# Kernel tuning notes

Measured on AMD Instinct MI355X. Metric: run time of the kernel, lower is better.

Reference implementation:

```python
import jax, jax.numpy as jnp
import numpy as np
from jax import lax


def _phi(x):
    # feature map phi(x) = elu(x) + 1 (non-negative)
    return jax.nn.elu(x) + 1.0


def setup_inputs() -> dict:
    key = jax.random.key(0)
    ks = jax.random.split(key, 5)
    B, T, D, H = 8, 4096, 1024, 64
    x = jax.random.normal(ks[0], (B, T, D), dtype=jnp.float32)
    # torch Linear(d_model, d_head, bias=False): y = x @ W.T; store as (in, out)
    W_q = jax.random.normal(ks[1], (D, H), dtype=jnp.float32) * (1.0 / np.sqrt(D))
    W_k = jax.random.normal(ks[2], (D, H), dtype=jnp.float32) * (1.0 / np.sqrt(D))
    W_v = jax.random.normal(ks[3], (D, H), dtype=jnp.float32) * (1.0 / np.sqrt(D))
    W_o = jax.random.normal(ks[4], (H, D), dtype=jnp.float32) * (1.0 / np.sqrt(H))
    return {"x": x, "W_q": W_q, "W_k": W_k, "W_v": W_v, "W_o": W_o}


def reference(x, W_q, W_k, W_v, W_o):
    B, T, D = x.shape
    H = W_q.shape[1]
    q = _phi(jnp.einsum('btd,dh->bth', x, W_q))  # [B,T,H]
    k = _phi(jnp.einsum('btd,dh->bth', x, W_k))
    v = jnp.einsum('btd,dh->bth', x, W_v)

    # time-major for scan: [T,B,H]
    qT = jnp.swapaxes(q, 0, 1)
    kT = jnp.swapaxes(k, 0, 1)
    vT = jnp.swapaxes(v, 0, 1)

    S0 = jnp.zeros((B, H, H), dtype=x.dtype)
    z0 = jnp.zeros((B, H), dtype=x.dtype)

    def step(carry, inp):
        S, z = carry
        q_t, k_t, v_t = inp
        S = S + k_t[:, :, None] * v_t[:, None, :]   # S += phi(k) v^T
        z = z + k_t
        o_t = jnp.einsum('bij,bj->bi', S, q_t)       # matches torch einsum exactly
        denom = jnp.maximum(jnp.sum(z * q_t, axis=-1, keepdims=True), 1e-6)
        return (S, z), o_t / denom

    (_, _), oT = lax.scan(step, (S0, z0), (qT, kT, vT))  # oT: [T,B,H]
    o = jnp.swapaxes(oT, 0, 1)                            # [B,T,H]
    # dropout is identity at inference
    return jnp.einsum('bth,hd->btd', o, W_o)
```

## Files before the change

### kernel.cpp

```cpp
#include <hip/hip_runtime.h>
#include <math.h>

typedef float4 f4;
typedef __attribute__((ext_vector_type(4))) float f32x4;
typedef __attribute__((ext_vector_type(8))) short short8;
typedef __attribute__((ext_vector_type(4))) unsigned short u16x4;

static constexpr int kB  = 8;
static constexpr int kT  = 4096;
static constexpr int kD  = 1024;
static constexpr int kH  = 64;
static constexpr int kC  = 64;
static constexpr int kNC = kT / kC;
static constexpr long kBT = (long)kB * kT;

__device__ __forceinline__ float phi_f(float x) {
    return x > 0.0f ? x + 1.0f : __expf(x);
}

__device__ __forceinline__ unsigned short f2bf(float f) {
    unsigned int u = __float_as_uint(f);
    u += 0x7FFF + ((u >> 16) & 1);
    return (unsigned short)(u >> 16);
}

typedef const __attribute__((address_space(1))) unsigned int gu32;
typedef __attribute__((address_space(3))) unsigned int lu32;
#define GLL16(SRC, DST) __builtin_amdgcn_global_load_lds((gu32*)(SRC), (lu32*)(DST), 16, 0, 0)

#define LD4F(dst, src) { f4 _t_ = *(const f4*)(src); (dst)[0]=_t_.x; (dst)[1]=_t_.y; (dst)[2]=_t_.z; (dst)[3]=_t_.w; }

__global__ __launch_bounds__(256)
void k0_prep(const float* __restrict__ Wq, const float* __restrict__ Wk,
             const float* __restrict__ Wv, const float* __restrict__ Wo,
             unsigned short* __restrict__ Wg, unsigned short* __restrict__ Wot)
{
    int g = blockIdx.x * 256 + threadIdx.x;
    if (g < 24576) {
        int r   = g % 192;
        int rem = g / 192;
        int c   = rem & 3;
        int kt  = rem >> 2;
        int mat = r >> 6, nn = r & 63;
        const float* W = (mat == 0) ? Wq : ((mat == 1) ? Wk : Wv);
        int kbase = kt * 32 + c * 8;
        unsigned short* dst = Wg + (long)g * 8;
        #pragma unroll
        for (int e = 0; e < 8; ++e) dst[e] = f2bf(W[(long)(kbase + e) * kH + nn]);
    } else if (g < 24576 + 4096) {
        int g2 = g - 24576;
        int n  = g2 >> 2;
        int kc = (g2 & 3) * 16;
        unsigned short* dst = Wot + n * kH + kc;
        #pragma unroll
        for (int i = 0; i < 16; ++i) dst[i] = f2bf(Wo[(long)(kc + i) * kD + n]);
    }
}

__global__ __launch_bounds__(256, 2)
void k1_qkv_mfma(const float* __restrict__ x, const unsigned short* __restrict__ Wg,
                 float* __restrict__ q, float* __restrict__ k, float* __restrict__ v)
{
    __shared__ unsigned short Bs[2][6144];
    __shared__ unsigned short As[2][2048];

    const int t = threadIdx.x;
    const int w = t >> 6;
    const int l = t & 63;
    const long mb = (long)blockIdx.x * 64;

    const int arow = t >> 2;
    const int ac   = t & 3;
    const float* ap = x + (mb + arow) * kD + ac * 8;
    const int awoff = (ac * 64 + arow) * 8;

    const int fc = l >> 4;
    const int fr = l & 15;

    f32x4 acc[12];
    #pragma unroll
    for (int i = 0; i < 12; ++i) acc[i] = (f32x4){0.f, 0.f, 0.f, 0.f};

    #pragma unroll
    for (int c3 = 0; c3 < 3; ++c3) {
        int idx = w * 3 + c3;
        GLL16(Wg + idx * 512 + l * 8, &Bs[0][idx * 512]);
    }
    f32x4 a0 = *(const f32x4*)ap;
    f32x4 a1 = *(const f32x4*)(ap + 4);
    {
        short8 ab;
        ab[0] = (short)f2bf(a0[0]); ab[1] = (short)f2bf(a0[1]);
        ab[2] = (short)f2bf(a0[2]); ab[3] = (short)f2bf(a0[3]);
        ab[4] = (short)f2bf(a1[0]); ab[5] = (short)f2bf(a1[1]);
        ab[6] = (short)f2bf(a1[2]); ab[7] = (short)f2bf(a1[3]);
        *(short8*)&As[0][awoff] = ab;
    }
    a0 = *(const f32x4*)(ap + 32);
    a1 = *(const f32x4*)(ap + 36);
    __syncthreads();

    for (int kt = 0; kt < 32; ++kt) {
        const int cur = kt & 1, nxt = cur ^ 1;
        if (kt + 1 < 32) {
            #pragma unroll
            for (int c3 = 0; c3 < 3; ++c3) {
                int idx = w * 3 + c3;
                GLL16(Wg + (long)(kt + 1) * 6144 + idx * 512 + l * 8, &Bs[nxt][idx * 512]);
            }
            short8 ab;
            ab[0] = (short)f2bf(a0[0]); ab[1] = (short)f2bf(a0[1]);
            ab[2] = (short)f2bf(a0[2]); ab[3] = (short)f2bf(a0[3]);
            ab[4] = (short)f2bf(a1[0]); ab[5] = (short)f2bf(a1[1]);
            ab[6] = (short)f2bf(a1[2]); ab[7] = (short)f2bf(a1[3]);
            *(short8*)&As[nxt][awoff] = ab;
            if (kt + 2 < 32) {
                a0 = *(const f32x4*)(ap + (kt + 2) * 32);
                a1 = *(const f32x4*)(ap + (kt + 2) * 32 + 4);
            }
        }
        short8 af = *(const short8*)&As[cur][(fc * 64 + w * 16 + fr) * 8];
        #pragma unroll
        for (int n16 = 0; n16 < 12; ++n16) {
            short8 bf = *(const short8*)&Bs[cur][(fc * 192 + n16 * 16 + fr) * 8];
            acc[n16] = __builtin_amdgcn_mfma_f32_16x16x32_bf16(af, bf, acc[n16], 0, 0, 0);
        }
        __syncthreads();
    }

    const int om = (l >> 4) * 4;
    #pragma unroll
    for (int n16 = 0; n16 < 12; ++n16) {
        int mat = n16 >> 2;
        int col = (n16 & 3) * 16 + (l & 15);
        float* outp = (mat == 0) ? q : ((mat == 1) ? k : v);
        #pragma unroll
        for (int reg = 0; reg < 4; ++reg) {
            long row = mb + w * 16 + om + reg;
            float val = acc[n16][reg];
            if (mat < 2) val = phi_f(val);
            outp[row * kH + col] = val;
        }
    }
}

__global__ __launch_bounds__(256)
void k2_state(const float* __restrict__ k, const float* __restrict__ v,
              float* __restrict__ Sc, float* __restrict__ zc)
{
    __shared__ float Ks2[64][64];
    __shared__ float Vs2[64][64];
    const int t = threadIdx.x;
    const long bc = blockIdx.x;
    const long rowbase = bc * kC;

    #pragma unroll
    for (int i = 0; i < 4; ++i) {
        int fi  = t + i * 256;
        int tau = fi >> 4;
        int cc  = (fi & 15) * 4;
        *(f4*)&Ks2[tau][cc] = *(const f4*)&k[(rowbase + tau) * kH + cc];
        *(f4*)&Vs2[tau][cc] = *(const f4*)&v[(rowbase + tau) * kH + cc];
    }
    __syncthreads();

    const int i  = t >> 2;
    const int j0 = (t & 3) * 16;
    float acc[16];
    #pragma unroll
    for (int c = 0; c < 16; ++c) acc[c] = 0.0f;
    float zacc = 0.0f;

    for (int tau = 0; tau < 64; ++tau) {
        float kv = Ks2[tau][i];
        zacc += kv;
        #pragma unroll
        for (int c = 0; c < 4; ++c) {
            float vv[4];
            LD4F(vv, &Vs2[tau][j0 + c * 4]);
            #pragma unroll
            for (int e = 0; e < 4; ++e) acc[c * 4 + e] += kv * vv[e];
        }
    }
    float* scp = Sc + bc * (kH * kH) + i * kH + j0;
    #pragma unroll
    for (int c = 0; c < 4; ++c) {
        f4 val; val.x = acc[c*4]; val.y = acc[c*4+1]; val.z = acc[c*4+2]; val.w = acc[c*4+3];
        *(f4*)&scp[c * 4] = val;
    }
    if ((t & 3) == 0) zc[bc * kH + i] = zacc;
}

__global__ __launch_bounds__(256)
void k3_prefix(const float* __restrict__ Sc, float* __restrict__ Sp,
               const float* __restrict__ zc, float* __restrict__ zp)
{
    const int t = threadIdx.x;
    const int blk = blockIdx.x;
    if (blk < 128) {
        int g = blk * 256 + t;
        int b = g >> 12;
        int rem = g & 4095;
        const float* src = Sc + (long)b * kNC * kH * kH + rem;
        float*       dst = Sp + (long)b * kNC * kH * kH + rem;
        float vals[kNC];
        #pragma unroll
        for (int c = 0; c < kNC; ++c) vals[c] = src[c * (kH * kH)];
        float run = 0.0f;
        #pragma unroll
        for (int c = 0; c < kNC; ++c) { float nv = vals[c]; vals[c] = run; run += nv; }
        #pragma unroll
        for (int c = 0; c < kNC; ++c) dst[c * (kH * kH)] = vals[c];
    } else {
        int g = (blk - 128) * 256 + t;
        int b = g >> 6;
        int i = g & 63;
        const float* src = zc + (long)b * kNC * kH + i;
        float*       dst = zp + (long)b * kNC * kH + i;
        float vals[kNC];
        #pragma unroll
        for (int c = 0; c < kNC; ++c) vals[c] = src[c * kH];
        float run = 0.0f;
        #pragma unroll
        for (int c = 0; c < kNC; ++c) { float nv = vals[c]; vals[c] = run; run += nv; }
        #pragma unroll
        for (int c = 0; c < kNC; ++c) dst[c * kH] = vals[c];
    }
}

__global__ __launch_bounds__(256)
void k4_chunkout(const float* __restrict__ q, const float* __restrict__ k,
                 const float* __restrict__ v, const float* __restrict__ Sp,
                 const float* __restrict__ zp, unsigned short* __restrict__ o)
{
    __shared__ float QT[64 * 64];
    __shared__ float KsS[64 * 64];
    __shared__ float VT[64 * 64];
    __shared__ float zps[64];
    __shared__ float ds[64];

    const int t = threadIdx.x;
    const long bc = blockIdx.x;
    const long rowbase = bc * kC;

    #pragma unroll
    for (int ii = 0; ii < 4; ++ii) {
        int fi  = t + ii * 256;
        int tau = fi >> 4;
        int c4  = fi & 15;
        f4 qv = *(const f4*)&q[(rowbase + tau) * kH + c4 * 4];
        QT[(c4 * 4 + 0) * 64 + tau] = qv.x;
        QT[(c4 * 4 + 1) * 64 + tau] = qv.y;
        QT[(c4 * 4 + 2) * 64 + tau] = qv.z;
        QT[(c4 * 4 + 3) * 64 + tau] = qv.w;
        f4 vv = *(const f4*)&v[(rowbase + tau) * kH + c4 * 4];
        VT[(c4 * 4 + 0) * 64 + tau] = vv.x;
        VT[(c4 * 4 + 1) * 64 + tau] = vv.y;
        VT[(c4 * 4 + 2) * 64 + tau] = vv.z;
        VT[(c4 * 4 + 3) * 64 + tau] = vv.w;
        f4 kv = *(const f4*)&k[(rowbase + tau) * kH + c4 * 4];
        *(f4*)&KsS[tau * 64 + 4 * (c4 ^ (tau & 15))] = kv;
    }
    if (t < 16) {
        *(f4*)&zps[t * 4] = *(const f4*)&zp[bc * kH + t * 4];
    }
    __syncthreads();

    const int tg   = t & 15;
    const int ig   = t >> 4;
    const int tau0 = tg * 4;
    const int ip0  = ig * 4;

    float pv[4][4];
    #pragma unroll
    for (int a = 0; a < 4; ++a)
        #pragma unroll
        for (int b2 = 0; b2 < 4; ++b2) pv[a][b2] = 0.0f;
    for (int xx = 0; xx < 64; ++xx) {
        float q4[4], v4[4];
        LD4F(q4, &QT[xx * 64 + tau0]);
        LD4F(v4, &VT[xx * 64 + ip0]);
        #pragma unroll
        for (int e1 = 0; e1 < 4; ++e1)
            #pragma unroll
            for (int e0 = 0; e0 < 4; ++e0) pv[e1][e0] += v4[e1] * q4[e0];
    }
    __syncthreads();
    #pragma unroll
    for (int e1 = 0; e1 < 4; ++e1) {
        int tp = ip0 + e1;
        f4 w;
        w.x = (tp <= tau0 + 0) ? pv[e1][0] : 0.0f;
        w.y = (tp <= tau0 + 1) ? pv[e1][1] : 0.0f;
        w.z = (tp <= tau0 + 2) ? pv[e1][2] : 0.0f;
        w.w = (tp <= tau0 + 3) ? pv[e1][3] : 0.0f;
        *(f4*)&VT[tp * 64 + tau0] = w;
    }
    __syncthreads();

    float acc[4][4];
    #pragma unroll
    for (int a = 0; a < 4; ++a)
        #pragma unroll
        for (int b2 = 0; b2 < 4; ++b2) acc[a][b2] = 0.0f;
    for (int tp = 0; tp < 64; ++tp) {
        float p4[4], k4[4];
        LD4F(p4, &VT[tp * 64 + tau0]);
        LD4F(k4, &KsS[tp * 64 + 4 * (ig ^ (tp & 15))]);
        #pragma unroll
        for (int e0 = 0; e0 < 4; ++e0)
            #pragma unroll
            for (int e1 = 0; e1 < 4; ++e1) acc[e0][e1] += p4[e0] * k4[e1];
    }
    __syncthreads();

    #pragma unroll
    for (int ii = 0; ii < 4; ++ii) {
        int fi = t + ii * 256;
        int ir = fi >> 4;
        int j4 = fi & 15;
        f4 sv = *(const f4*)&Sp[bc * (kH * kH) + ir * kH + j4 * 4];
        VT[(j4 * 4 + 0) * 64 + ir] = sv.x;
        VT[(j4 * 4 + 1) * 64 + ir] = sv.y;
        VT[(j4 * 4 + 2) * 64 + ir] = sv.z;
        VT[(j4 * 4 + 3) * 64 + ir] = sv.w;
    }
    if (t < 64) {
        float run = 0.0f;
        const int jc4 = t >> 2, jr = t & 3;
        for (int tau = 0; tau < 64; ++tau) {
            int idx = tau * 64 + 4 * (jc4 ^ (tau & 15)) + jr;
            run += KsS[idx];
            KsS[idx] = run;
        }
    }
    __syncthreads();

    if (t < 64) {
        float dacc = 0.0f;
        for (int j = 0; j < 64; ++j) {
            float qv = QT[j * 64 + t];
            float ck = KsS[t * 64 + 4 * ((j >> 2) ^ (t & 15)) + (j & 3)];
            dacc += qv * (ck + zps[j]);
        }
        ds[t] = 1.0f / fmaxf(dacc, 1e-6f);
    }

    for (int j = 0; j < 64; ++j) {
        float q4[4], s4[4];
        LD4F(q4, &QT[j * 64 + tau0]);
        LD4F(s4, &VT[j * 64 + ip0]);
        #pragma unroll
        for (int e0 = 0; e0 < 4; ++e0)
            #pragma unroll
            for (int e1 = 0; e1 < 4; ++e1) acc[e0][e1] += q4[e0] * s4[e1];
    }
    __syncthreads();

    #pragma unroll
    for (int e0 = 0; e0 < 4; ++e0) {
        float inv = ds[tau0 + e0];
        u16x4 wv;
        wv[0] = f2bf(acc[e0][0] * inv);
        wv[1] = f2bf(acc[e0][1] * inv);
        wv[2] = f2bf(acc[e0][2] * inv);
        wv[3] = f2bf(acc[e0][3] * inv);
        *(u16x4*)&o[(rowbase + tau0 + e0) * kH + ip0] = wv;
    }
}

__global__ __launch_bounds__(256, 4)
void k5_outproj_mfma(const unsigned short* __restrict__ o,
                     const unsigned short* __restrict__ Wot,
                     float* __restrict__ out)
{
    __shared__ unsigned short Os[128 * 64];
    __shared__ unsigned short Ws5[128 * 64];
    const int t = threadIdx.x;
    const int w = t >> 6, l = t & 63;
    const int wm = w >> 1, wn = w & 1;
    const int mb = blockIdx.x >> 3;
    const int nb = blockIdx.x & 7;
    const long row0 = (long)mb * 128;
    const int  col0 = nb * 128;

    const int rin = l >> 3;
    const int cch = l & 7;
    #pragma unroll
    for (int c = 0; c < 4; ++c) {
        int r = (c * 4 + w) * 8 + rin;
        int g = cch ^ (r & 7);
        GLL16(o   + (row0 + r) * kH + g * 8,        Os  + (c * 4 + w) * 512);
        GLL16(Wot + (long)(col0 + r) * kH + g * 8,  Ws5 + (c * 4 + w) * 512);
    }
    __syncthreads();

    short8 af[4][2];
    #pragma unroll
    for (int mf = 0; mf < 4; ++mf) {
        int ar = wm * 64 + mf * 16 + (l & 15);
        #pragma unroll
        for (int ks = 0; ks < 2; ++ks)
            af[mf][ks] = *(const short8*)(Os + ar * 64 + (((ks * 4 + (l >> 4)) ^ (ar & 7)) * 8));
    }

    f32x4 acc[4][4];
    #pragma unroll
    for (int a = 0; a < 4; ++a)
        #pragma unroll
        for (int b2 = 0; b2 < 4; ++b2) acc[a][b2] = (f32x4){0.f, 0.f, 0.f, 0.f};

    #pragma unroll
    for (int nf = 0; nf < 4; ++nf) {
        int br = wn * 64 + nf * 16 + (l & 15);
        short8 bf0 = *(const short8*)(Ws5 + br * 64 + ((((l >> 4)) ^ (br & 7)) * 8));
        short8 bf1 = *(const short8*)(Ws5 + br * 64 + (((4 + (l >> 4)) ^ (br & 7)) * 8));
        #pragma unroll
        for (int mf = 0; mf < 4; ++mf) {
            acc[mf][nf] = __builtin_amdgcn_mfma_f32_16x16x32_bf16(af[mf][0], bf0, acc[mf][nf], 0, 0, 0);
            acc[mf][nf] = __builtin_amdgcn_mfma_f32_16x16x32_bf16(af[mf][1], bf1, acc[mf][nf], 0, 0, 0);
        }
    }

    #pragma unroll
    for (int mf = 0; mf < 4; ++mf)
        #pragma unroll
        for (int nf = 0; nf < 4; ++nf) {
            #pragma unroll
            for (int reg = 0; reg < 4; ++reg) {
                long row = row0 + wm * 64 + mf * 16 + (l >> 4) * 4 + reg;
                int  col = col0 + wn * 64 + nf * 16 + (l & 15);
                out[row * kD + col] = acc[mf][nf][reg];
            }
        }
}

extern "C" void kernel_launch(void* const* d_in, const int* in_sizes, int n_in,
                              void* d_out, int out_size, void* d_ws, size_t ws_size,
                              hipStream_t stream)
{
    const float* x  = (const float*)d_in[0];
    const float* Wq = (const float*)d_in[1];
    const float* Wk = (const float*)d_in[2];
    const float* Wv = (const float*)d_in[3];
    const float* Wo = (const float*)d_in[4];
    float* out = (float*)d_out;
    float* ws  = (float*)d_ws;

    const long NQ = kBT * kH;
    float* q  = ws;
    float* k  = ws + NQ;
    float* v  = ws + 2 * NQ;
    float* Sc = ws + 3 * NQ;
    float* Sp = ws + 4 * NQ;
    unsigned short* obf = (unsigned short*)(ws + 5 * NQ);
    float* zc = ws + 5 * NQ + NQ / 2;
    float* zp = zc + (long)kB * kNC * kH;
    unsigned short* Wg  = (unsigned short*)(zp + (long)kB * kNC * kH);
    unsigned short* Wot = Wg + 192 * 1024;

    k0_prep<<<112, 256, 0, stream>>>(Wq, Wk, Wv, Wo, Wg, Wot);
    k1_qkv_mfma<<<512, 256, 0, stream>>>(x, Wg, q, k, v);
    k2_state<<<kB * kNC, 256, 0, stream>>>(k, v, Sc, zc);
    k3_prefix<<<130, 256, 0, stream>>>(Sc, Sp, zc, zp);
    k4_chunkout<<<kB * kNC, 256, 0, stream>>>(q, k, v, Sp, zp, obf);
    k5_outproj_mfma<<<2048, 256, 0, stream>>>(obf, Wot, out);
}
```

Before: 307.3 us.

## Rewrite intra-chunk output kernel with bf16 MFMA and split-bf16 prefix state

The chunk output kernel, previously scalar FP32 FMAs over LDS, is replaced by bf16 MFMA matmuls for QK^T, QV^T-style masked products and Q·S. The QKV projection kernel now also emits bf16 copies of q/k/v and a transposed k tile. The prefix-sum kernel writes the state as a high/low bf16 pair to keep it close to fp32 precision. Inputs are staged into LDS with direct global-to-LDS loads. In exchange the intra-chunk terms run in bf16 (accuracy risk), and the extra bf16 buffers add memory writes.

```diff
diff --git a/kernel.cpp b/kernel.cpp
--- a/kernel.cpp
+++ b/kernel.cpp
@@ -4,7 +4,7 @@
 typedef float4 f4;
 typedef __attribute__((ext_vector_type(4))) float f32x4;
 typedef __attribute__((ext_vector_type(8))) short short8;
-typedef __attribute__((ext_vector_type(4))) unsigned short u16x4;
+typedef __attribute__((ext_vector_type(8))) unsigned short u16x8;
 
 static constexpr int kB  = 8;
 static constexpr int kT  = 4096;
@@ -22,6 +22,10 @@
     unsigned int u = __float_as_uint(f);
     u += 0x7FFF + ((u >> 16) & 1);
     return (unsigned short)(u >> 16);
+}
+
+__device__ __forceinline__ float bf2f(unsigned short u) {
+    return __uint_as_float((unsigned int)u << 16);
 }
 
 typedef const __attribute__((address_space(1))) unsigned int gu32;
@@ -59,7 +63,10 @@
 
 __global__ __launch_bounds__(256, 2)
 void k1_qkv_mfma(const float* __restrict__ x, const unsigned short* __restrict__ Wg,
-                 float* __restrict__ q, float* __restrict__ k, float* __restrict__ v)
+                 unsigned short* __restrict__ qb,
+                 float* __restrict__ kf, unsigned short* __restrict__ kb,
+                 float* __restrict__ vf, unsigned short* __restrict__ vb,
+                 unsigned short* __restrict__ kTg)
 {
     __shared__ unsigned short Bs[2][6144];
     __shared__ unsigned short As[2][2048];
@@ -128,19 +135,39 @@
         __syncthreads();
     }
 
+    unsigned short* kTt = &Bs[0][0];
     const int om = (l >> 4) * 4;
     #pragma unroll
     for (int n16 = 0; n16 < 12; ++n16) {
         int mat = n16 >> 2;
         int col = (n16 & 3) * 16 + (l & 15);
-        float* outp = (mat == 0) ? q : ((mat == 1) ? k : v);
         #pragma unroll
         for (int reg = 0; reg < 4; ++reg) {
-            long row = mb + w * 16 + om + reg;
+            int  row  = w * 16 + om + reg;
+            long grow = mb + row;
             float val = acc[n16][reg];
             if (mat < 2) val = phi_f(val);
-            outp[row * kH + col] = val;
-        }
+            unsigned short bv = f2bf(val);
+            if (mat == 0) {
+                qb[grow * kH + col] = bv;
+            } else if (mat == 1) {
+                kf[grow * kH + col] = val;
+                kb[grow * kH + col] = bv;
+                kTt[col * 72 + row] = bv;
+            } else {
+                vf[grow * kH + col] = val;
+                vb[grow * kH + col] = bv;
+            }
+        }
+    }
+    __syncthreads();
+    {
+        int i = t >> 2, s = (t & 3) * 16;
+        u16x8 h0 = *(const u16x8*)&kTt[i * 72 + s];
+        u16x8 h1 = *(const u16x8*)&kTt[i * 72 + s + 8];
+        unsigned short* dst = kTg + (long)blockIdx.x * 4096 + i * 64 + s;
+        *(u16x8*)dst       = h0;
+        *(u16x8*)(dst + 8) = h1;
     }
 }
 
@@ -192,7 +219,8 @@
 }
 
 __global__ __launch_bounds__(256)
-void k3_prefix(const float* __restrict__ Sc, float* __restrict__ Sp,
+void k3_prefix(const float* __restrict__ Sc,
+               unsigned short* __restrict__ SpH, unsigned short* __restrict__ SpL,
                const float* __restrict__ zc, float* __restrict__ zp)
 {
     const int t = threadIdx.x;
@@ -201,16 +229,21 @@
         int g = blk * 256 + t;
         int b = g >> 12;
         int rem = g & 4095;
-        const float* src = Sc + (long)b * kNC * kH * kH + rem;
-        float*       dst = Sp + (long)b * kNC * kH * kH + rem;
+        const float* src       = Sc  + (long)b * kNC * 4096 + rem;
+        unsigned short* dh     = SpH + (long)b * kNC * 4096 + rem;
+        unsigned short* dl     = SpL + (long)b * kNC * 4096 + rem;
         float vals[kNC];
         #pragma unroll
-        for (int c = 0; c < kNC; ++c) vals[c] = src[c * (kH * kH)];
+        for (int c = 0; c < kNC; ++c) vals[c] = src[c * 4096];
         float run = 0.0f;
         #pragma unroll
         for (int c = 0; c < kNC; ++c) { float nv = vals[c]; vals[c] = run; run += nv; }
         #pragma unroll
-        for (int c = 0; c < kNC; ++c) dst[c * (kH * kH)] = vals[c];
+        for (int c = 0; c < kNC; ++c) {
+            unsigned short h = f2bf(vals[c]);
+            dh[c * 4096] = h;
+            dl[c * 4096] = f2bf(vals[c] - bf2f(h));
+        }
     } else {
         int g = (blk - 128) * 256 + t;
         int b = g >> 6;
@@ -228,144 +261,122 @@
     }
 }
 
-__global__ __launch_bounds__(256)
-void k4_chunkout(const float* __restrict__ q, const float* __restrict__ k,
-                 const float* __restrict__ v, const float* __restrict__ Sp,
-                 const float* __restrict__ zp, unsigned short* __restrict__ o)
-{
-    __shared__ float QT[64 * 64];
-    __shared__ float KsS[64 * 64];
-    __shared__ float VT[64 * 64];
-    __shared__ float zps[64];
-    __shared__ float ds[64];
+__global__ __launch_bounds__(256, 2)
+void k4_chunkout_mfma(const unsigned short* __restrict__ qb,
+                      const unsigned short* __restrict__ kb,
+                      const unsigned short* __restrict__ vb,
+                      const unsigned short* __restrict__ kTg,
+                      const unsigned short* __restrict__ SpH,
+                      const unsigned short* __restrict__ SpL,
+                      const float* __restrict__ zp,
+                      unsigned short* __restrict__ o)
+{
+    __shared__ unsigned short Q[4096], K[4096], V[4096], KT[4096];
+    __shared__ unsigned short SH[4096], SL[4096], Pl[4096];
+    __shared__ float zps[64], qz[64];
 
     const int t = threadIdx.x;
+    const int w = t >> 6, l = t & 63;
     const long bc = blockIdx.x;
-    const long rowbase = bc * kC;
-
-    #pragma unroll
-    for (int ii = 0; ii < 4; ++ii) {
-        int fi  = t + ii * 256;
-        int tau = fi >> 4;
-        int c4  = fi & 15;
-        f4 qv = *(const f4*)&q[(rowbase + tau) * kH + c4 * 4];
-        QT[(c4 * 4 + 0) * 64 + tau] = qv.x;
-        QT[(c4 * 4 + 1) * 64 + tau] = qv.y;
-        QT[(c4 * 4 + 2) * 64 + tau] = qv.z;
-        QT[(c4 * 4 + 3) * 64 + tau] = qv.w;
-        f4 vv = *(const f4*)&v[(rowbase + tau) * kH + c4 * 4];
-        VT[(c4 * 4 + 0) * 64 + tau] = vv.x;
-        VT[(c4 * 4 + 1) * 64 + tau] = vv.y;
-        VT[(c4 * 4 + 2) * 64 + tau] = vv.z;
-        VT[(c4 * 4 + 3) * 64 + tau] = vv.w;
-        f4 kv = *(const f4*)&k[(rowbase + tau) * kH + c4 * 4];
-        *(f4*)&KsS[tau * 64 + 4 * (c4 ^ (tau & 15))] = kv;
-    }
-    if (t < 16) {
-        *(f4*)&zps[t * 4] = *(const f4*)&zp[bc * kH + t * 4];
-    }
-    __syncthreads();
-
-    const int tg   = t & 15;
-    const int ig   = t >> 4;
-    const int tau0 = tg * 4;
-    const int ip0  = ig * 4;
-
-    float pv[4][4];
-    #pragma unroll
-    for (int a = 0; a < 4; ++a)
-        #pragma unroll
-        for (int b2 = 0; b2 < 4; ++b2) pv[a][b2] = 0.0f;
-    for (int xx = 0; xx < 64; ++xx) {
-        float q4[4], v4[4];
-        LD4F(q4, &QT[xx * 64 + tau0]);
-        LD4F(v4, &VT[xx * 64 + ip0]);
-        #pragma unroll
-        for (int e1 = 0; e1 < 4; ++e1)
-            #pragma unroll
-            for (int e0 = 0; e0 < 4; ++e0) pv[e1][e0] += v4[e1] * q4[e0];
-    }
-    __syncthreads();
-    #pragma unroll
-    for (int e1 = 0; e1 < 4; ++e1) {
-        int tp = ip0 + e1;
-        f4 w;
-        w.x = (tp <= tau0 + 0) ? pv[e1][0] : 0.0f;
-        w.y = (tp <= tau0 + 1) ? pv[e1][1] : 0.0f;
-        w.z = (tp <= tau0 + 2) ? pv[e1][2] : 0.0f;
-        w.w = (tp <= tau0 + 3) ? pv[e1][3] : 0.0f;
-        *(f4*)&VT[tp * 64 + tau0] = w;
-    }
-    __syncthreads();
-
-    float acc[4][4];
-    #pragma unroll
-    for (int a = 0; a < 4; ++a)
-        #pragma unroll
-        for (int b2 = 0; b2 < 4; ++b2) acc[a][b2] = 0.0f;
-    for (int tp = 0; tp < 64; ++tp) {
-        float p4[4], k4[4];
-        LD4F(p4, &VT[tp * 64 + tau0]);
-        LD4F(k4, &KsS[tp * 64 + 4 * (ig ^ (tp & 15))]);
-        #pragma unroll
-        for (int e0 = 0; e0 < 4; ++e0)
-            #pragma unroll
-            for (int e1 = 0; e1 < 4; ++e1) acc[e0][e1] += p4[e0] * k4[e1];
-    }
-    __syncthreads();
-
-    #pragma unroll
-    for (int ii = 0; ii < 4; ++ii) {
-        int fi = t + ii * 256;
-        int ir = fi >> 4;
-        int j4 = fi & 15;
-        f4 sv = *(const f4*)&Sp[bc * (kH * kH) + ir * kH + j4 * 4];
-        VT[(j4 * 4 + 0) * 64 + ir] = sv.x;
-        VT[(j4 * 4 + 1) * 64 + ir] = sv.y;
-        VT[(j4 * 4 + 2) * 64 + ir] = sv.z;
-        VT[(j4 * 4 + 3) * 64 + ir] = sv.w;
+    const long base = bc * 4096;
+
+    #pragma unroll
+    for (int j2 = 0; j2 < 2; ++j2) {
+        int j = w * 2 + j2;
+        int off = j * 512 + l * 8;
+        GLL16(qb  + base + off, Q  + j * 512);
+        GLL16(kb  + base + off, K  + j * 512);
+        GLL16(vb  + base + off, V  + j * 512);
+        GLL16(kTg + base + off, KT + j * 512);
+        GLL16(SpH + base + off, SH + j * 512);
+        GLL16(SpL + base + off, SL + j * 512);
+    }
+    if (t < 16) *(f4*)&zps[t * 4] = *(const f4*)&zp[bc * kH + t * 4];
+    __syncthreads();
+
+    const int fr = l & 15, fc = l >> 4;
+    const int aoff = (w * 16 + fr) * 64 + fc * 8;
+
+    f32x4 s_acc[4], p_acc[4];
+    #pragma unroll
+    for (int n16 = 0; n16 < 4; ++n16) {
+        s_acc[n16] = (f32x4){0.f, 0.f, 0.f, 0.f};
+        p_acc[n16] = (f32x4){0.f, 0.f, 0.f, 0.f};
+    }
+    #pragma unroll
+    for (int k32 = 0; k32 < 2; ++k32) {
+        short8 aq = *(const short8*)&Q[aoff + k32 * 32];
+        #pragma unroll
+        for (int n16 = 0; n16 < 4; ++n16) {
+            int boff = (n16 * 16 + fr) * 64 + k32 * 32 + fc * 8;
+            s_acc[n16] = __builtin_amdgcn_mfma_f32_16x16x32_bf16(
+                aq, *(const short8*)&K[boff], s_acc[n16], 0, 0, 0);
+            p_acc[n16] = __builtin_amdgcn_mfma_f32_16x16x32_bf16(
+                aq, *(const short8*)&V[boff], p_acc[n16], 0, 0, 0);
+        }
+    }
+
+    float rsum[4] = {0.f, 0.f, 0.f, 0.f};
+    #pragma unroll
+    for (int n16 = 0; n16 < 4; ++n16) {
+        int col = n16 * 16 + fr;
+        #pragma unroll
+        for (int reg = 0; reg < 4; ++reg) {
+            int row = w * 16 + fc * 4 + reg;
+            bool keep = (col <= row);
+            Pl[row * 64 + col] = keep ? f2bf(p_acc[n16][reg]) : (unsigned short)0;
+            if (keep) rsum[reg] += s_acc[n16][reg];
+        }
+    }
+    #pragma unroll
+    for (int reg = 0; reg < 4; ++reg) {
+        rsum[reg] += __shfl_xor(rsum[reg], 1);
+        rsum[reg] += __shfl_xor(rsum[reg], 2);
+        rsum[reg] += __shfl_xor(rsum[reg], 4);
+        rsum[reg] += __shfl_xor(rsum[reg], 8);
     }
     if (t < 64) {
-        float run = 0.0f;
-        const int jc4 = t >> 2, jr = t & 3;
-        for (int tau = 0; tau < 64; ++tau) {
-            int idx = tau * 64 + 4 * (jc4 ^ (tau & 15)) + jr;
-            run += KsS[idx];
-            KsS[idx] = run;
-        }
-    }
-    __syncthreads();
-
-    if (t < 64) {
-        float dacc = 0.0f;
-        for (int j = 0; j < 64; ++j) {
-            float qv = QT[j * 64 + t];
-            float ck = KsS[t * 64 + 4 * ((j >> 2) ^ (t & 15)) + (j & 3)];
-            dacc += qv * (ck + zps[j]);
-        }
-        ds[t] = 1.0f / fmaxf(dacc, 1e-6f);
-    }
-
-    for (int j = 0; j < 64; ++j) {
-        float q4[4], s4[4];
-        LD4F(q4, &QT[j * 64 + tau0]);
-        LD4F(s4, &VT[j * 64 + ip0]);
-        #pragma unroll
-        for (int e0 = 0; e0 < 4; ++e0)
-            #pragma unroll
-            for (int e1 = 0; e1 < 4; ++e1) acc[e0][e1] += q4[e0] * s4[e1];
-    }
-    __syncthreads();
-
-    #pragma unroll
-    for (int e0 = 0; e0 < 4; ++e0) {
-        float inv = ds[tau0 + e0];
-        u16x4 wv;
-        wv[0] = f2bf(acc[e0][0] * inv);
-        wv[1] = f2bf(acc[e0][1] * inv);
-        wv[2] = f2bf(acc[e0][2] * inv);
-        wv[3] = f2bf(acc[e0][3] * inv);
-        *(u16x4*)&o[(rowbase + tau0 + e0) * kH + ip0] = wv;
+        float accz = 0.0f;
+        #pragma unroll 8
+        for (int j = 0; j < 64; ++j) accz += bf2f(Q[t * 64 + j]) * zps[j];
+        qz[t] = accz;
+    }
+    __syncthreads();
+
+    f32x4 o_acc[4];
+    #pragma unroll
+    for (int n16 = 0; n16 < 4; ++n16) o_acc[n16] = (f32x4){0.f, 0.f, 0.f, 0.f};
+    #pragma unroll
+    for (int k32 = 0; k32 < 2; ++k32) {
+        short8 ap = *(const short8*)&Pl[aoff + k32 * 32];
+        short8 aq = *(const short8*)&Q[aoff + k32 * 32];
+        #pragma unroll
+        for (int n16 = 0; n16 < 4; ++n16) {
+            int boff = (n16 * 16 + fr) * 64 + k32 * 32 + fc * 8;
+            o_acc[n16] = __builtin_amdgcn_mfma_f32_16x16x32_bf16(
+                ap, *(const short8*)&KT[boff], o_acc[n16], 0, 0, 0);
+            o_acc[n16] = __builtin_amdgcn_mfma_f32_16x16x32_bf16(
+                aq, *(const short8*)&SH[boff], o_acc[n16], 0, 0, 0);
+            o_acc[n16] = __builtin_amdgcn_mfma_f32_16x16x32_bf16(
+                aq, *(const short8*)&SL[boff], o_acc[n16], 0, 0, 0);
+        }
+    }
+
+    float invd[4];
+    #pragma unroll
+    for (int reg = 0; reg < 4; ++reg) {
+        int row = w * 16 + fc * 4 + reg;
+        invd[reg] = 1.0f / fmaxf(rsum[reg] + qz[row], 1e-6f);
+    }
+    const long rowg = bc * 64;
+    #pragma unroll
+    for (int n16 = 0; n16 < 4; ++n16) {
+        int col = n16 * 16 + fr;
+        #pragma unroll
+        for (int reg = 0; reg < 4; ++reg) {
+            int row = w * 16 + fc * 4 + reg;
+            o[(rowg + row) * kH + col] = f2bf(o_acc[n16][reg] * invd[reg]);
+        }
     }
 }
 
@@ -448,21 +459,25 @@
     float* ws  = (float*)d_ws;
 
     const long NQ = kBT * kH;
-    float* q  = ws;
-    float* k  = ws + NQ;
-    float* v  = ws + 2 * NQ;
-    float* Sc = ws + 3 * NQ;
-    float* Sp = ws + 4 * NQ;
-    unsigned short* obf = (unsigned short*)(ws + 5 * NQ);
-    float* zc = ws + 5 * NQ + NQ / 2;
+    float* kf = ws;
+    float* vf = ws + NQ;
+    float* Sc = ws + 2 * NQ;
+    float* zc = ws + 3 * NQ;
     float* zp = zc + (long)kB * kNC * kH;
-    unsigned short* Wg  = (unsigned short*)(zp + (long)kB * kNC * kH);
+    unsigned short* qb  = (unsigned short*)(zp + (long)kB * kNC * kH);
+    unsigned short* kb  = qb  + NQ;
+    unsigned short* vb  = kb  + NQ;
+    unsigned short* kTg = vb  + NQ;
+    unsigned short* SpH = kTg + NQ;
+    unsigned short* SpL = SpH + NQ;
+    unsigned short* obf = SpL + NQ;
+    unsigned short* Wg  = obf + NQ;
     unsigned short* Wot = Wg + 192 * 1024;
 
     k0_prep<<<112, 256, 0, stream>>>(Wq, Wk, Wv, Wo, Wg, Wot);
-    k1_qkv_mfma<<<512, 256, 0, stream>>>(x, Wg, q, k, v);
-    k2_state<<<kB * kNC, 256, 0, stream>>>(k, v, Sc, zc);
-    k3_prefix<<<130, 256, 0, stream>>>(Sc, Sp, zc, zp);
-    k4_chunkout<<<kB * kNC, 256, 0, stream>>>(q, k, v, Sp, zp, obf);
+    k1_qkv_mfma<<<512, 256, 0, stream>>>(x, Wg, qb, kf, kb, vf, vb, kTg);
+    k2_state<<<kB * kNC, 256, 0, stream>>>(kf, vf, Sc, zc);
+    k3_prefix<<<130, 256, 0, stream>>>(Sc, SpH, SpL, zc, zp);
+    k4_chunkout_mfma<<<kB * kNC, 256, 0, stream>>>(qb, kb, vb, kTg, SpH, SpL, zp, obf);
     k5_outproj_mfma<<<2048, 256, 0, stream>>>(obf, Wot, out);
 }
```

After: 301.0 us. 1.02x faster.
